# Kernel optimization log

Measured on AMD Instinct MI355X. Metric: run time of the kernel, lower is better.

Reference implementation:

```python
import jax, jax.numpy as jnp
import numpy as np

OBS_DIM = 512
ATTN_DIM = 128


def setup_inputs() -> dict:
    key = jax.random.key(0)
    k1, k2, k3, k4 = jax.random.split(key, 4)
    agent_observation = jax.random.normal(k1, (128, 32, 512), dtype=jnp.float32)
    visible_observations = jax.random.normal(k2, (128, 32, 16, 512), dtype=jnp.float32)
    # learned bilinear projection params (match torch.randn init)
    w_psi = jax.random.normal(k3, (OBS_DIM, ATTN_DIM), dtype=jnp.float32)
    w_phi = jax.random.normal(k4, (OBS_DIM, ATTN_DIM), dtype=jnp.float32)
    return {
        "agent_observation": agent_observation,
        "visible_observations": visible_observations,
        "w_psi": w_psi,
        "w_phi": w_phi,
    }


def reference(agent_observation, visible_observations, w_psi, w_phi):
    # beta[b,e,a] = agent_obs[b,e] @ W_psi @ W_phi^T @ visible[b,e,a]
    q = jnp.einsum("bed,dk->bek", agent_observation, w_psi)          # (B,E,K)
    kv = jnp.einsum("bead,dk->beak", visible_observations, w_phi)    # (B,E,A,K)
    betas = jnp.einsum("bek,beak->bea", q, kv)                       # (B,E,A)
    # softmax over the visible-agent axis (the inner loop axis, dim=1 of
    # the per-entity stacked beta matrix in the original code)
    return jax.nn.softmax(betas, axis=-1)
```

## Files before the change

kernel.cpp:

```cpp
#include <hip/hip_runtime.h>
#include <math.h>

#define OBS 512
#define ATT 128
#define NA 16
#define RPB 8

__global__ void transpose_wphi_k(const float* __restrict__ wphi,
                                 float* __restrict__ wphiT) {
  int idx = blockIdx.x * 256 + threadIdx.x;
  int k  = idx >> 9;
  int dd = idx & 511;
  wphiT[idx] = wphi[dd * ATT + k];
}

__device__ __forceinline__ void fma4(float4& acc, float a, float4 w) {
  acc.x = fmaf(a, w.x, acc.x);
  acc.y = fmaf(a, w.y, acc.y);
  acc.z = fmaf(a, w.z, acc.z);
  acc.w = fmaf(a, w.w, acc.w);
}

__launch_bounds__(256)
__global__ void entity_attn_k(const float* __restrict__ A,
                              const float* __restrict__ V,
                              const float* __restrict__ Wpsi,
                              const float* __restrict__ WphiT,
                              float* __restrict__ Out)
{
  __shared__ __align__(16) float qtS[ATT * RPB];
  __shared__ __align__(16) float regB[12288];

  const int tid  = threadIdx.x;
  const int lane = tid & 63;
  const int wave = tid >> 6;
  const int g0   = blockIdx.x * RPB;

  {
    const int r  = tid & 7;
    const int c  = tid >> 3;
    const int d0 = c * 16;
    const float4* arow = (const float4*)(A + (size_t)(g0 + r) * OBS + d0);
    float4 v0 = arow[0], v1 = arow[1], v2 = arow[2], v3 = arow[3];
    float tmp[16] = {v0.x,v0.y,v0.z,v0.w, v1.x,v1.y,v1.z,v1.w,
                     v2.x,v2.y,v2.z,v2.w, v3.x,v3.y,v3.z,v3.w};
#pragma unroll
    for (int j = 0; j < 16; ++j) regB[(d0 + j) * 8 + r] = tmp[j];
  }
  __syncthreads();

  {
    const int kg = tid & 31;
    const int ds = tid >> 5;
    const int k0 = kg * 4;
    const int dbase = ds * 64;
    float4 acc[8];
#pragma unroll
    for (int r = 0; r < 8; ++r) acc[r] = make_float4(0.f, 0.f, 0.f, 0.f);
    const float4* wp4 = (const float4*)Wpsi;
#pragma unroll 4
    for (int i = 0; i < 64; ++i) {
      const int d = dbase + i;
      float4 w = wp4[d * 32 + kg];
      const float4* at4 = (const float4*)(regB + d * 8);
      float4 a01 = at4[0];
      float4 a23 = at4[1];
      fma4(acc[0], a01.x, w); fma4(acc[1], a01.y, w);
      fma4(acc[2], a01.z, w); fma4(acc[3], a01.w, w);
      fma4(acc[4], a23.x, w); fma4(acc[5], a23.y, w);
      fma4(acc[6], a23.z, w); fma4(acc[7], a23.w, w);
    }
    float4* qp4 = (float4*)regB;
#pragma unroll
    for (int r = 0; r < 8; ++r)
      qp4[(4096 + (ds * 8 + r) * 128 + k0) >> 2] = acc[r];
  }
  __syncthreads();

  {
    const int r  = tid & 7;
    const int kq = tid >> 3;
    const int k0 = kq * 4;
    const float4* qp4 = (const float4*)regB;
    float4 s = make_float4(0.f, 0.f, 0.f, 0.f);
#pragma unroll
    for (int ds = 0; ds < 8; ++ds) {
      float4 p = qp4[(4096 + (ds * 8 + r) * 128 + k0) >> 2];
      s.x += p.x; s.y += p.y; s.z += p.z; s.w += p.w;
    }
    qtS[(k0 + 0) * 8 + r] = s.x;
    qtS[(k0 + 1) * 8 + r] = s.y;
    qtS[(k0 + 2) * 8 + r] = s.z;
    qtS[(k0 + 3) * 8 + r] = s.w;
  }
  __syncthreads();

  {
    const int kh  = wave & 1;
    const int ddh = wave >> 1;
    const int dd0 = ddh * 256 + lane * 4;
    const int kq  = kh * 64 + lane;
    const float4* qt4 = (const float4*)qtS;
    float4 qa = qt4[kq * 2];
    float4 qb = qt4[kq * 2 + 1];
    float q8[8] = {qa.x, qa.y, qa.z, qa.w, qb.x, qb.y, qb.z, qb.w};
    float4 acc[8];
#pragma unroll
    for (int r = 0; r < 8; ++r) acc[r] = make_float4(0.f, 0.f, 0.f, 0.f);
    const float4* wt4 = (const float4*)WphiT;
#pragma unroll 4
    for (int kk = 0; kk < 64; ++kk) {
      const int k = kh * 64 + kk;
      float4 wt = wt4[(k * 512 + dd0) >> 2];
#pragma unroll
      for (int r = 0; r < 8; ++r) {
        float qv = __shfl(q8[r], kk, 64);
        fma4(acc[r], qv, wt);
      }
    }
    float4* up4 = (float4*)regB;
#pragma unroll
    for (int r = 0; r < 8; ++r)
      up4[((kh * 8 + r) * 512 + dd0) >> 2] = acc[r];
  }
  __syncthreads();

  {
    const int r   = tid >> 5;
    const int dd0 = (tid & 31) * 16;
    const float4* up4 = (const float4*)regB;
    float4* u4 = (float4*)(regB + 8192);
#pragma unroll
    for (int seg = 0; seg < 4; ++seg) {
      const int o = r * 512 + dd0 + seg * 4;
      float4 x = up4[o >> 2];
      float4 y = up4[(4096 + o) >> 2];
      x.x += y.x; x.y += y.y; x.z += y.z; x.w += y.w;
      u4[o >> 2] = x;
    }
  }
  __syncthreads();

  const float* u = regB + 8192;
  const float4* V4 = (const float4*)V;
#pragma unroll
  for (int rr = 0; rr < 2; ++rr) {
    const int r = wave * 2 + rr;
    const size_t g = (size_t)(g0 + r);
    const float4* vrow = V4 + g * 2048;
    const float4* ur = (const float4*)(u + r * 512);
    float4 uf0 = ur[lane * 2];
    float4 uf1 = ur[lane * 2 + 1];
    float acc[16];
#pragma unroll
    for (int a = 0; a < 16; ++a) {
      float4 v0 = vrow[a * 128 + lane * 2];
      float4 v1 = vrow[a * 128 + lane * 2 + 1];
      float s;
      s = uf0.x * v0.x;
      s = fmaf(uf0.y, v0.y, s);
      s = fmaf(uf0.z, v0.z, s);
      s = fmaf(uf0.w, v0.w, s);
      s = fmaf(uf1.x, v1.x, s);
      s = fmaf(uf1.y, v1.y, s);
      s = fmaf(uf1.z, v1.z, s);
      s = fmaf(uf1.w, v1.w, s);
      acc[a] = s;
    }
#pragma unroll
    for (int a = 0; a < 16; ++a) {
      float v = acc[a];
      v += __shfl_xor(v, 32, 64);
      v += __shfl_xor(v, 16, 64);
      v += __shfl_xor(v,  8, 64);
      v += __shfl_xor(v,  4, 64);
      v += __shfl_xor(v,  2, 64);
      v += __shfl_xor(v,  1, 64);
      acc[a] = v;
    }
    float mx = acc[0];
#pragma unroll
    for (int a = 1; a < 16; ++a) mx = fmaxf(mx, acc[a]);
    float ssum = 0.f;
#pragma unroll
    for (int a = 0; a < 16; ++a) { acc[a] = __expf(acc[a] - mx); ssum += acc[a]; }
    const float inv = 1.0f / ssum;
    if (lane == 0) {
      float4* o4 = (float4*)(Out + g * 16);
      o4[0] = make_float4(acc[0]  * inv, acc[1]  * inv, acc[2]  * inv, acc[3]  * inv);
      o4[1] = make_float4(acc[4]  * inv, acc[5]  * inv, acc[6]  * inv, acc[7]  * inv);
      o4[2] = make_float4(acc[8]  * inv, acc[9]  * inv, acc[10] * inv, acc[11] * inv);
      o4[3] = make_float4(acc[12] * inv, acc[13] * inv, acc[14] * inv, acc[15] * inv);
    }
  }
}

extern "C" void kernel_launch(void* const* d_in, const int* in_sizes, int n_in,
                              void* d_out, int out_size, void* d_ws, size_t ws_size,
                              hipStream_t stream) {
  (void)in_sizes; (void)n_in; (void)out_size; (void)ws_size;
  const float* A    = (const float*)d_in[0];
  const float* V    = (const float*)d_in[1];
  const float* Wpsi = (const float*)d_in[2];
  const float* Wphi = (const float*)d_in[3];
  float* Out = (float*)d_out;
  float* WphiT = (float*)d_ws;

  transpose_wphi_k<<<256, 256, 0, stream>>>(Wphi, WphiT);
  entity_attn_k<<<512, 256, 0, stream>>>(A, V, Wpsi, WphiT, Out);
}
```

Before: 50.98 us.

## Halve rows per block, shrink shared memory, restructure projection stages for occupancy

After: 52.11 us. +2.2%, slower.

```diff
diff --git a/kernel.cpp b/kernel.cpp
--- a/kernel.cpp
+++ b/kernel.cpp
@@ -3,8 +3,7 @@
 
 #define OBS 512
 #define ATT 128
-#define NA 16
-#define RPB 8
+#define RPB 4
 
 __global__ void transpose_wphi_k(const float* __restrict__ wphi,
                                  float* __restrict__ wphiT) {
@@ -14,22 +13,21 @@
   wphiT[idx] = wphi[dd * ATT + k];
 }
 
-__device__ __forceinline__ void fma4(float4& acc, float a, float4 w) {
-  acc.x = fmaf(a, w.x, acc.x);
-  acc.y = fmaf(a, w.y, acc.y);
-  acc.z = fmaf(a, w.z, acc.z);
-  acc.w = fmaf(a, w.w, acc.w);
+__device__ __forceinline__ void fma4(float4& a, float s, float4 w) {
+  a.x = fmaf(s, w.x, a.x);
+  a.y = fmaf(s, w.y, a.y);
+  a.z = fmaf(s, w.z, a.z);
+  a.w = fmaf(s, w.w, a.w);
 }
 
-__launch_bounds__(256)
+__launch_bounds__(256, 4)
 __global__ void entity_attn_k(const float* __restrict__ A,
                               const float* __restrict__ V,
                               const float* __restrict__ Wpsi,
                               const float* __restrict__ WphiT,
                               float* __restrict__ Out)
 {
-  __shared__ __align__(16) float qtS[ATT * RPB];
-  __shared__ __align__(16) float regB[12288];
+  __shared__ __align__(16) float S[6656];
 
   const int tid  = threadIdx.x;
   const int lane = tid & 63;
@@ -37,135 +35,111 @@
   const int g0   = blockIdx.x * RPB;
 
   {
-    const int r  = tid & 7;
-    const int c  = tid >> 3;
-    const int d0 = c * 16;
-    const float4* arow = (const float4*)(A + (size_t)(g0 + r) * OBS + d0);
-    float4 v0 = arow[0], v1 = arow[1], v2 = arow[2], v3 = arow[3];
-    float tmp[16] = {v0.x,v0.y,v0.z,v0.w, v1.x,v1.y,v1.z,v1.w,
-                     v2.x,v2.y,v2.z,v2.w, v3.x,v3.y,v3.z,v3.w};
-#pragma unroll
-    for (int j = 0; j < 16; ++j) regB[(d0 + j) * 8 + r] = tmp[j];
+    const int r = tid & 3;
+    const int c = tid >> 2;
+    const float4* a4 = (const float4*)(A + (size_t)(g0 + r) * OBS) + c * 2;
+    float4 v0 = a4[0], v1 = a4[1];
+    const int d0 = c * 8;
+    S[(d0+0)*4+r] = v0.x; S[(d0+1)*4+r] = v0.y;
+    S[(d0+2)*4+r] = v0.z; S[(d0+3)*4+r] = v0.w;
+    S[(d0+4)*4+r] = v1.x; S[(d0+5)*4+r] = v1.y;
+    S[(d0+6)*4+r] = v1.z; S[(d0+7)*4+r] = v1.w;
   }
   __syncthreads();
 
   {
     const int kg = tid & 31;
     const int ds = tid >> 5;
-    const int k0 = kg * 4;
+    float4 acc0 = make_float4(0.f,0.f,0.f,0.f);
+    float4 acc1 = acc0, acc2 = acc0, acc3 = acc0;
+    const float4* wp4 = (const float4*)Wpsi;
+    const float4* at4 = (const float4*)S;
     const int dbase = ds * 64;
-    float4 acc[8];
-#pragma unroll
-    for (int r = 0; r < 8; ++r) acc[r] = make_float4(0.f, 0.f, 0.f, 0.f);
-    const float4* wp4 = (const float4*)Wpsi;
-#pragma unroll 4
+#pragma unroll 8
     for (int i = 0; i < 64; ++i) {
       const int d = dbase + i;
       float4 w = wp4[d * 32 + kg];
-      const float4* at4 = (const float4*)(regB + d * 8);
-      float4 a01 = at4[0];
-      float4 a23 = at4[1];
-      fma4(acc[0], a01.x, w); fma4(acc[1], a01.y, w);
-      fma4(acc[2], a01.z, w); fma4(acc[3], a01.w, w);
-      fma4(acc[4], a23.x, w); fma4(acc[5], a23.y, w);
-      fma4(acc[6], a23.z, w); fma4(acc[7], a23.w, w);
+      float4 a = at4[d];
+      fma4(acc0, a.x, w);
+      fma4(acc1, a.y, w);
+      fma4(acc2, a.z, w);
+      fma4(acc3, a.w, w);
     }
-    float4* qp4 = (float4*)regB;
-#pragma unroll
-    for (int r = 0; r < 8; ++r)
-      qp4[(4096 + (ds * 8 + r) * 128 + k0) >> 2] = acc[r];
+    float4* qp4 = (float4*)(S + 2048);
+    qp4[(ds*4+0)*32 + kg] = acc0;
+    qp4[(ds*4+1)*32 + kg] = acc1;
+    qp4[(ds*4+2)*32 + kg] = acc2;
+    qp4[(ds*4+3)*32 + kg] = acc3;
   }
   __syncthreads();
 
   {
-    const int r  = tid & 7;
-    const int kq = tid >> 3;
-    const int k0 = kq * 4;
-    const float4* qp4 = (const float4*)regB;
-    float4 s = make_float4(0.f, 0.f, 0.f, 0.f);
 #pragma unroll
-    for (int ds = 0; ds < 8; ++ds) {
-      float4 p = qp4[(4096 + (ds * 8 + r) * 128 + k0) >> 2];
-      s.x += p.x; s.y += p.y; s.z += p.z; s.w += p.w;
+    for (int e = tid; e < 512; e += 256) {
+      const int r = e & 3;
+      const int k = e >> 2;
+      float s = 0.f;
+#pragma unroll
+      for (int ds = 0; ds < 8; ++ds) s += S[2048 + (ds*4 + r)*128 + k];
+      S[6144 + k*4 + r] = s;
     }
-    qtS[(k0 + 0) * 8 + r] = s.x;
-    qtS[(k0 + 1) * 8 + r] = s.y;
-    qtS[(k0 + 2) * 8 + r] = s.z;
-    qtS[(k0 + 3) * 8 + r] = s.w;
   }
   __syncthreads();
 
   {
-    const int kh  = wave & 1;
-    const int ddh = wave >> 1;
-    const int dd0 = ddh * 256 + lane * 4;
-    const int kq  = kh * 64 + lane;
-    const float4* qt4 = (const float4*)qtS;
-    float4 qa = qt4[kq * 2];
-    float4 qb = qt4[kq * 2 + 1];
-    float q8[8] = {qa.x, qa.y, qa.z, qa.w, qb.x, qb.y, qb.z, qb.w};
-    float4 acc[8];
+    float acc[8] = {0.f,0.f,0.f,0.f,0.f,0.f,0.f,0.f};
+    const float4* qt4 = (const float4*)(S + 6144);
+#pragma unroll 4
+    for (int k = 0; k < 128; ++k) {
+      float w0 = WphiT[k*512 + tid];
+      float w1 = WphiT[k*512 + tid + 256];
+      float4 q = qt4[k];
+      acc[0] = fmaf(q.x, w0, acc[0]);
+      acc[1] = fmaf(q.y, w0, acc[1]);
+      acc[2] = fmaf(q.z, w0, acc[2]);
+      acc[3] = fmaf(q.w, w0, acc[3]);
+      acc[4] = fmaf(q.x, w1, acc[4]);
+      acc[5] = fmaf(q.y, w1, acc[5]);
+      acc[6] = fmaf(q.z, w1, acc[6]);
+      acc[7] = fmaf(q.w, w1, acc[7]);
+    }
 #pragma unroll
-    for (int r = 0; r < 8; ++r) acc[r] = make_float4(0.f, 0.f, 0.f, 0.f);
-    const float4* wt4 = (const float4*)WphiT;
-#pragma unroll 4
-    for (int kk = 0; kk < 64; ++kk) {
-      const int k = kh * 64 + kk;
-      float4 wt = wt4[(k * 512 + dd0) >> 2];
-#pragma unroll
-      for (int r = 0; r < 8; ++r) {
-        float qv = __shfl(q8[r], kk, 64);
-        fma4(acc[r], qv, wt);
-      }
+    for (int r = 0; r < 4; ++r) {
+      S[r*512 + tid]       = acc[r];
+      S[r*512 + tid + 256] = acc[4+r];
     }
-    float4* up4 = (float4*)regB;
-#pragma unroll
-    for (int r = 0; r < 8; ++r)
-      up4[((kh * 8 + r) * 512 + dd0) >> 2] = acc[r];
   }
   __syncthreads();
 
   {
-    const int r   = tid >> 5;
-    const int dd0 = (tid & 31) * 16;
-    const float4* up4 = (const float4*)regB;
-    float4* u4 = (float4*)(regB + 8192);
-#pragma unroll
-    for (int seg = 0; seg < 4; ++seg) {
-      const int o = r * 512 + dd0 + seg * 4;
-      float4 x = up4[o >> 2];
-      float4 y = up4[(4096 + o) >> 2];
-      x.x += y.x; x.y += y.y; x.z += y.z; x.w += y.w;
-      u4[o >> 2] = x;
-    }
-  }
-  __syncthreads();
-
-  const float* u = regB + 8192;
-  const float4* V4 = (const float4*)V;
-#pragma unroll
-  for (int rr = 0; rr < 2; ++rr) {
-    const int r = wave * 2 + rr;
+    const int r = wave;
     const size_t g = (size_t)(g0 + r);
-    const float4* vrow = V4 + g * 2048;
-    const float4* ur = (const float4*)(u + r * 512);
-    float4 uf0 = ur[lane * 2];
-    float4 uf1 = ur[lane * 2 + 1];
+    const float4* vrow = (const float4*)V + g * 2048;
+    const float4* ur   = (const float4*)S + r * 128;
+    const float4 uf0 = ur[lane*2];
+    const float4 uf1 = ur[lane*2 + 1];
     float acc[16];
 #pragma unroll
-    for (int a = 0; a < 16; ++a) {
-      float4 v0 = vrow[a * 128 + lane * 2];
-      float4 v1 = vrow[a * 128 + lane * 2 + 1];
-      float s;
-      s = uf0.x * v0.x;
-      s = fmaf(uf0.y, v0.y, s);
-      s = fmaf(uf0.z, v0.z, s);
-      s = fmaf(uf0.w, v0.w, s);
-      s = fmaf(uf1.x, v1.x, s);
-      s = fmaf(uf1.y, v1.y, s);
-      s = fmaf(uf1.z, v1.z, s);
-      s = fmaf(uf1.w, v1.w, s);
-      acc[a] = s;
+    for (int ag = 0; ag < 4; ++ag) {
+      float4 va[8];
+#pragma unroll
+      for (int j = 0; j < 4; ++j) {
+        va[j*2]   = vrow[(ag*4 + j)*128 + lane*2];
+        va[j*2+1] = vrow[(ag*4 + j)*128 + lane*2 + 1];
+      }
+#pragma unroll
+      for (int j = 0; j < 4; ++j) {
+        float s;
+        s = uf0.x * va[j*2].x;
+        s = fmaf(uf0.y, va[j*2].y, s);
+        s = fmaf(uf0.z, va[j*2].z, s);
+        s = fmaf(uf0.w, va[j*2].w, s);
+        s = fmaf(uf1.x, va[j*2+1].x, s);
+        s = fmaf(uf1.y, va[j*2+1].y, s);
+        s = fmaf(uf1.z, va[j*2+1].z, s);
+        s = fmaf(uf1.w, va[j*2+1].w, s);
+        acc[ag*4 + j] = s;
+      }
     }
 #pragma unroll
     for (int a = 0; a < 16; ++a) {
@@ -187,10 +161,10 @@
     const float inv = 1.0f / ssum;
     if (lane == 0) {
       float4* o4 = (float4*)(Out + g * 16);
-      o4[0] = make_float4(acc[0]  * inv, acc[1]  * inv, acc[2]  * inv, acc[3]  * inv);
-      o4[1] = make_float4(acc[4]  * inv, acc[5]  * inv, acc[6]  * inv, acc[7]  * inv);
-      o4[2] = make_float4(acc[8]  * inv, acc[9]  * inv, acc[10] * inv, acc[11] * inv);
-      o4[3] = make_float4(acc[12] * inv, acc[13] * inv, acc[14] * inv, acc[15] * inv);
+      o4[0] = make_float4(acc[0]*inv,  acc[1]*inv,  acc[2]*inv,  acc[3]*inv);
+      o4[1] = make_float4(acc[4]*inv,  acc[5]*inv,  acc[6]*inv,  acc[7]*inv);
+      o4[2] = make_float4(acc[8]*inv,  acc[9]*inv,  acc[10]*inv, acc[11]*inv);
+      o4[3] = make_float4(acc[12]*inv, acc[13]*inv, acc[14]*inv, acc[15]*inv);
     }
   }
 }
@@ -203,9 +177,9 @@
   const float* V    = (const float*)d_in[1];
   const float* Wpsi = (const float*)d_in[2];
   const float* Wphi = (const float*)d_in[3];
-  float* Out = (float*)d_out;
+  float* Out   = (float*)d_out;
   float* WphiT = (float*)d_ws;
 
   transpose_wphi_k<<<256, 256, 0, stream>>>(Wphi, WphiT);
-  entity_attn_k<<<512, 256, 0, stream>>>(A, V, Wpsi, WphiT, Out);
+  entity_attn_k<<<1024, 256, 0, stream>>>(A, V, Wpsi, WphiT, Out);
 }
```
